# Kernel optimization log

Hardware: AMD Instinct MI355X
Metric: run time of the kernel (lower is better)

## Reference

```python
import jax, jax.numpy as jnp
import numpy as np

BLOCK = 128  # RHT block size (multiple of E8 lattice dim 8)


def _hadamard(n: int) -> np.ndarray:
    """Sylvester Hadamard matrix of size n (n power of 2), unnormalized."""
    H = np.array([[1.0]], dtype=np.float32)
    while H.shape[0] < n:
        H = np.block([[H, H], [H, -H]]).astype(np.float32)
    return H

_H = jnp.asarray(_hadamard(BLOCK) / np.sqrt(BLOCK))  # orthonormal [BLOCK, BLOCK]


def rht(x, signs):
    """Block-diagonal randomized Hadamard transform: x*signs then blockwise H.
    x: [T, D] with D % BLOCK == 0; signs: [D] of +-1."""
    T, D = x.shape
    xs = (x * signs).reshape(T, D // BLOCK, BLOCK)
    return jnp.einsum('tnb,bc->tnc', xs, _H).reshape(T, D)


def e8rht_linear(x, wq, scale, signs):
    """E8RHT quantized linear: rotate input, dequantize weight, matmul.
    wq: [out, in] quantized codes (stored as float), scale: [out] per-row scale."""
    xr = rht(x, signs)                       # [T, in]
    w = wq * scale[:, None]                  # dequantize [out, in]
    return xr @ w.T                          # [T, out]


def setup_inputs() -> dict:
    key = jax.random.key(0)
    ks = jax.random.split(key, 7)
    T, D_IN, D_MID, D_OUT = 16384, 1024, 4096, 1024
    x = jax.random.normal(ks[0], (T, D_IN), dtype=jnp.float32)
    # simulate lattice-quantized codes: small-integer-ish values
    up_wq = jnp.round(jax.random.normal(ks[1], (D_MID, D_IN)) * 2.0)
    up_scale = (jax.random.uniform(ks[2], (D_MID,)) * 0.02 + 0.005).astype(jnp.float32)
    down_wq = jnp.round(jax.random.normal(ks[3], (D_OUT, D_MID)) * 2.0)
    down_scale = (jax.random.uniform(ks[4], (D_OUT,)) * 0.02 + 0.005).astype(jnp.float32)
    up_signs = jnp.sign(jax.random.normal(ks[5], (D_IN,))).astype(jnp.float32)
    down_signs = jnp.sign(jax.random.normal(ks[6], (D_MID,))).astype(jnp.float32)
    return {"x": x, "up_wq": up_wq, "up_scale": up_scale,
            "down_wq": down_wq, "down_scale": down_scale,
            "up_signs": up_signs, "down_signs": down_signs}


def reference(x, up_wq, up_scale, down_wq, down_scale, up_signs, down_signs):
    h = e8rht_linear(x, up_wq, up_scale, up_signs)       # [T, D_MID]
    a = jax.nn.gelu(h)                                    # non-gated activation
    out = e8rht_linear(a, down_wq, down_scale, down_signs)  # [T, D_OUT]
    return out
```

## Files before the change

kernel.cpp:

```cpp
#include <hip/hip_runtime.h>
#include <hip/hip_bf16.h>
#include <stdint.h>


typedef __attribute__((ext_vector_type(8))) short short8;
typedef __attribute__((ext_vector_type(16))) float floatx16;

__device__ __forceinline__ float bf2f(unsigned int u16) {
    union { unsigned int i; float f; } v;
    v.i = u16 << 16;
    return v.f;
}

__device__ __forceinline__ unsigned short f2bf(float f) {
    union { float f; unsigned int i; } v;
    v.f = f;
    unsigned int r = v.i + 0x7FFFu + ((v.i >> 16) & 1u);
    return (unsigned short)(r >> 16);
}

__device__ __forceinline__ float gelu_tanh(float x) {
    float u = 0.7978845608028654f * (x + 0.044715f * x * x * x);
    float e = __expf(2.0f * u);
    float t = 1.0f - 2.0f / (e + 1.0f);
    return 0.5f * x * (1.0f + t);
}

__device__ __forceinline__ int dtype_flag(const void* signs_raw) {
    return ((*(const unsigned int*)signs_raw) & 0xFFFFu) ? 1 : 0;
}

__device__ __forceinline__ void fwht_block(const void* wq, const void* scale,
                                           const void* signs, unsigned short* out,
                                           int fl, int D, int nblk, int gwave, int lane) {
    int o = gwave / nblk;
    int blk = gwave - o * nblk;
    size_t base = (size_t)o * D + (size_t)blk * 128;

    float v0, v1, s0, s1, sc;
    if (fl) {
        unsigned int p = ((const unsigned int*)((const unsigned short*)wq + base))[lane];
        v0 = bf2f(p & 0xffffu);
        v1 = bf2f(p >> 16);
        unsigned int sp =
            ((const unsigned int*)((const unsigned short*)signs + (size_t)blk * 128))[lane];
        s0 = bf2f(sp & 0xffffu);
        s1 = bf2f(sp >> 16);
        sc = bf2f(((const unsigned short*)scale)[o]);
    } else {
        const float* wf = (const float*)wq + base;
        v0 = wf[2 * lane];
        v1 = wf[2 * lane + 1];
        const float* sf = (const float*)signs + (size_t)blk * 128;
        s0 = sf[2 * lane];
        s1 = sf[2 * lane + 1];
        sc = ((const float*)scale)[o];
    }

    {
        float a = v0, b = v1;
        v0 = a + b;
        v1 = a - b;
    }
#pragma unroll
    for (int m = 1; m <= 32; m <<= 1) {
        float p0 = __shfl_xor(v0, m, 64);
        float p1 = __shfl_xor(v1, m, 64);
        if (lane & m) {
            v0 = p0 - v0;
            v1 = p1 - v1;
        } else {
            v0 = v0 + p0;
            v1 = v1 + p1;
        }
    }

    sc *= 0.08838834764831845f;
    unsigned short o0 = f2bf(v0 * sc * s0);
    unsigned short o1 = f2bf(v1 * sc * s1);
    ((unsigned int*)(out + base))[lane] = (unsigned int)o0 | ((unsigned int)o1 << 16);
}

__global__ __launch_bounds__(256) void prep(const void* __restrict__ x,
                                            const void* __restrict__ up_wq,
                                            const void* __restrict__ up_scale,
                                            const void* __restrict__ dn_wq,
                                            const void* __restrict__ dn_scale,
                                            const void* __restrict__ up_signs,
                                            const void* __restrict__ dn_signs,
                                            unsigned short* __restrict__ x_bf,
                                            unsigned short* __restrict__ w_up,
                                            unsigned short* __restrict__ w_dn,
                                            int nbX, int nbW, int D_IN, int D_MID) {
    const int fl = dtype_flag(up_signs);
    const int bid = blockIdx.x;
    if (bid < nbX) {
        size_t e = ((size_t)bid * 256 + threadIdx.x) * 8;
        if (fl) {
            *(uint4*)(x_bf + e) = *(const uint4*)((const unsigned short*)x + e);
        } else {
            const float* xf = (const float*)x + e;
            uint4 r;
            r.x = (unsigned)f2bf(xf[0]) | ((unsigned)f2bf(xf[1]) << 16);
            r.y = (unsigned)f2bf(xf[2]) | ((unsigned)f2bf(xf[3]) << 16);
            r.z = (unsigned)f2bf(xf[4]) | ((unsigned)f2bf(xf[5]) << 16);
            r.w = (unsigned)f2bf(xf[6]) | ((unsigned)f2bf(xf[7]) << 16);
            *(uint4*)(x_bf + e) = r;
        }
    } else if (bid < nbX + nbW) {
        int gwave = (bid - nbX) * 4 + (threadIdx.x >> 6);
        fwht_block(up_wq, up_scale, up_signs, w_up, fl, D_IN, D_IN / 128, gwave,
                   threadIdx.x & 63);
    } else {
        int gwave = (bid - nbX - nbW) * 4 + (threadIdx.x >> 6);
        fwht_block(dn_wq, dn_scale, dn_signs, w_dn, fl, D_MID, D_MID / 128, gwave,
                   threadIdx.x & 63);
    }
}

template <int ACT, int OUT_DYN>
__global__ __launch_bounds__(256, 4) void gemm_bt(const unsigned short* __restrict__ A,
                                                  const unsigned short* __restrict__ B,
                                                  void* __restrict__ C,
                                                  const void* __restrict__ sflag,
                                                  int N, int K, int rowOff,
                                                  int NT, int GM, int strip) {
    __shared__ unsigned short As[128 * 32];
    __shared__ unsigned short Bs[128 * 32];

    int flat = blockIdx.x;
    int mt, nt;
    if (strip > 0) {
        int xcd = flat & 7;
        int s = flat >> 3;
        int perPanel = GM * NT;
        int p = s / perPanel;
        int r = s - p * perPanel;
        nt = r / GM;
        mt = xcd * strip + p * GM + (r - nt * GM);
    } else {
        int perPanel = GM * NT;
        int p = flat / perPanel;
        int r = flat - p * perPanel;
        nt = r / GM;
        mt = p * GM + (r - nt * GM);
    }
    const int tileM = mt * 128;
    const int tileN = nt * 128;

    const int tid = threadIdx.x;
    const int lane = tid & 63;
    const int wave = tid >> 6;
    const int fl = OUT_DYN ? dtype_flag(sflag) : 1;

    const int wm = wave & 1, wn = wave >> 1;
    const int m0 = wm * 64, n0 = wn * 64;

    const int srow = wave * 32 + (lane >> 2);
    const int scol = (((lane & 3) ^ ((srow >> 1) & 3)) * 8);

    floatx16 acc[2][2];
#pragma unroll
    for (int i = 0; i < 2; i++)
#pragma unroll
        for (int j = 0; j < 2; j++) acc[i][j] = (floatx16)0.0f;

    const int r31 = lane & 31;
    const int kg = lane >> 5;
    const int sl0 = kg ^ ((r31 >> 1) & 3);
    const int sl1 = sl0 ^ 2;

    const int eA[2][2] = {
        {(m0 + r31) * 32 + sl0 * 8, (m0 + r31) * 32 + sl1 * 8},
        {(m0 + 32 + r31) * 32 + sl0 * 8, (m0 + 32 + r31) * 32 + sl1 * 8}};
    const int eB[2][2] = {
        {(n0 + r31) * 32 + sl0 * 8, (n0 + r31) * 32 + sl1 * 8},
        {(n0 + 32 + r31) * 32 + sl0 * 8, (n0 + 32 + r31) * 32 + sl1 * 8}};

    const unsigned short* Abase = A + (size_t)(tileM + srow) * K + scol;
    const unsigned short* Bbase = B + (size_t)(tileN + srow) * K + scol;
    unsigned short* AsDst = As + wave * 1024;
    unsigned short* BsDst = Bs + wave * 1024;

    for (int k0 = 0; k0 < K; k0 += 32) {
        __builtin_amdgcn_global_load_lds(
            (const __attribute__((address_space(1))) unsigned int*)(Abase + k0),
            (__attribute__((address_space(3))) unsigned int*)(AsDst), 16, 0, 0);
        __builtin_amdgcn_global_load_lds(
            (const __attribute__((address_space(1))) unsigned int*)(Abase + k0 + (size_t)16 * K),
            (__attribute__((address_space(3))) unsigned int*)(AsDst + 512), 16, 0, 0);
        __builtin_amdgcn_global_load_lds(
            (const __attribute__((address_space(1))) unsigned int*)(Bbase + k0),
            (__attribute__((address_space(3))) unsigned int*)(BsDst), 16, 0, 0);
        __builtin_amdgcn_global_load_lds(
            (const __attribute__((address_space(1))) unsigned int*)(Bbase + k0 + (size_t)16 * K),
            (__attribute__((address_space(3))) unsigned int*)(BsDst + 512), 16, 0, 0);

        __syncthreads();

        short8 af[2][2], bf[2][2];
#pragma unroll
        for (int mi = 0; mi < 2; mi++)
#pragma unroll
            for (int ks = 0; ks < 2; ks++) {
                af[mi][ks] = *(const short8*)&As[eA[mi][ks]];
                bf[mi][ks] = *(const short8*)&Bs[eB[mi][ks]];
            }
#pragma unroll
        for (int mi = 0; mi < 2; mi++)
#pragma unroll
            for (int ni = 0; ni < 2; ni++)
#pragma unroll
                for (int ks = 0; ks < 2; ks++)
                    acc[mi][ni] = __builtin_amdgcn_mfma_f32_32x32x16_bf16(
                        af[mi][ks], bf[ni][ks], acc[mi][ni], 0, 0, 0);
        __syncthreads();
    }

#pragma unroll
    for (int mi = 0; mi < 2; mi++) {
        int rb0 = tileM + m0 + mi * 32 + kg * 4;
#pragma unroll
        for (int ni = 0; ni < 2; ni++) {
            int c = tileN + n0 + ni * 32 + r31;
#pragma unroll
            for (int g = 0; g < 4; g++) {
#pragma unroll
                for (int r = 0; r < 4; r++) {
                    float v = acc[mi][ni][g * 4 + r];
                    if (ACT) v = gelu_tanh(v);
                    size_t idx = (size_t)(rowOff + rb0 + g * 8 + r) * N + c;
                    if (fl)
                        ((unsigned short*)C)[idx] = f2bf(v);
                    else
                        ((float*)C)[idx] = v;
                }
            }
        }
    }
}

static inline int div_le(int n, int cap) {
    for (int g = cap; g > 1; --g)
        if (n % g == 0) return g;
    return 1;
}

extern "C" void kernel_launch(void* const* d_in, const int* in_sizes, int n_in,
                              void* d_out, int out_size, void* d_ws, size_t ws_size,
                              hipStream_t stream) {
    const int T = 16384, D_IN = 1024, D_MID = 4096, D_OUT = 1024;

    unsigned short* w_up = (unsigned short*)d_ws;
    unsigned short* w_dn = w_up + (size_t)D_MID * D_IN;
    unsigned short* x_bf = w_dn + (size_t)D_OUT * D_MID;
    unsigned short* a_buf = x_bf + (size_t)T * D_IN;

    size_t used = ((size_t)D_MID * D_IN + (size_t)D_OUT * D_MID + (size_t)T * D_IN) * 2;
    size_t avail = ws_size > used ? ws_size - used : 0;
    long tc = (long)(avail / ((size_t)D_MID * 2));
    tc = (tc / 128) * 128;
    if (tc > T) tc = T;
    if (tc < 128) tc = 128;
    const int Tc = (int)tc;

    {
        int nbX = (T * D_IN / 8) / 256;
        int nbW = (D_MID * (D_IN / 128)) / 4;
        prep<<<dim3(nbX + 2 * nbW), dim3(256), 0, stream>>>(
            d_in[0], d_in[1], d_in[2], d_in[3], d_in[4], d_in[5], d_in[6], x_bf, w_up, w_dn,
            nbX, nbW, D_IN, D_MID);
    }

    for (int r0 = 0; r0 < T; r0 += Tc) {
        int Ms = (T - r0 < Tc) ? (T - r0) : Tc;
        int MT = Ms / 128;
        int strip = (MT % 8 == 0) ? MT / 8 : 0;

        {
            int NT = D_MID / 128;
            int GM = (strip > 0) ? div_le(strip, 16) : div_le(MT, 4);
            gemm_bt<1, 0><<<dim3(MT * NT), dim3(256), 0, stream>>>(
                x_bf + (size_t)r0 * D_IN, w_up, a_buf, d_in[5], D_MID, D_IN, 0, NT, GM, strip);
        }
        {
            int NT = D_OUT / 128;
            int GM = (strip > 0) ? div_le(strip, 4) : div_le(MT, 4);
            gemm_bt<0, 1><<<dim3(MT * NT), dim3(256), 0, stream>>>(
                a_buf, w_dn, d_out, d_in[5], D_OUT, D_MID, r0, NT, GM, strip);
        }
    }
}
```

Before: 480.0 us.

## Replace 128x128 GEMM with 256x256 double-buffered 8-wave pipelined kernel

Replaces the simple single-buffered 128x128 tile GEMM (4 waves, 32x32 MFMA, BK=32) with a 256x256 tile kernel using 8 waves, 16x16x32 MFMA, BK=64 and double-buffered LDS. Global-to-LDS loads for the next K tile are interleaved between MFMA quadrants, with explicit waitcnt, barriers and setprio. The goal is to raise data reuse per byte loaded and hide load latency behind compute. In exchange it uses more LDS and registers, runs at lower occupancy, launches fewer blocks per GEMM, and relies on hand-placed barriers that are fragile.

Result: faster. 426.0 us (-11.2%).

```diff
diff --git a/kernel.cpp b/kernel.cpp
--- a/kernel.cpp
+++ b/kernel.cpp
@@ -1,10 +1,35 @@
 #include <hip/hip_runtime.h>
-#include <hip/hip_bf16.h>
 #include <stdint.h>
 
 
 typedef __attribute__((ext_vector_type(8))) short short8;
-typedef __attribute__((ext_vector_type(16))) float floatx16;
+typedef __attribute__((ext_vector_type(4))) float floatx4;
+
+#define GLOAD(gp, lp)                                                               \
+  __builtin_amdgcn_global_load_lds(                                                 \
+      (const __attribute__((address_space(1))) unsigned int*)(gp),                  \
+      (__attribute__((address_space(3))) unsigned int*)(lp), 16, 0, 0)
+
+#define SCHED0() __builtin_amdgcn_sched_barrier(0)
+#define BARRIER()                                  \
+  do {                                             \
+    SCHED0();                                      \
+    asm volatile("" ::: "memory");                 \
+    __builtin_amdgcn_s_barrier();                  \
+    asm volatile("" ::: "memory");                 \
+    SCHED0();                                      \
+  } while (0)
+#define LGKM0()                                              \
+  do {                                                       \
+    asm volatile("s_waitcnt lgkmcnt(0)" ::: "memory");       \
+    SCHED0();                                                \
+  } while (0)
+#define LGKM_HINT() asm volatile("s_waitcnt lgkmcnt(8)" ::: "memory")
+#define VMCNT(n)                                             \
+  do {                                                       \
+    asm volatile("s_waitcnt vmcnt(" #n ")" ::: "memory");    \
+    SCHED0();                                                \
+  } while (0)
 
 __device__ __forceinline__ float bf2f(unsigned int u16) {
     union { unsigned int i; float f; } v;
@@ -118,123 +143,180 @@
     }
 }
 
+__device__ __forceinline__ void stage_half(const unsigned short* g, unsigned short* l,
+                                           size_t goff, int K, int ldsW) {
+    GLOAD(g + goff, l + ldsW);
+    GLOAD(g + goff + (size_t)8 * K, l + ldsW + 512);
+}
+
+__device__ __forceinline__ void ld_frags(short8 (&fr)[2][2], const unsigned short* base,
+                                         int o0, int o1) {
+#pragma unroll
+    for (int f = 0; f < 2; ++f) {
+        fr[f][0] = *(const short8*)(base + f * 1024 + o0);
+        fr[f][1] = *(const short8*)(base + f * 1024 + o1);
+    }
+}
+
+__device__ __forceinline__ void ld_frags4(short8 (&fr)[4][2], const unsigned short* base,
+                                          int o0, int o1) {
+#pragma unroll
+    for (int f = 0; f < 4; ++f) {
+        fr[f][0] = *(const short8*)(base + f * 1024 + o0);
+        fr[f][1] = *(const short8*)(base + f * 1024 + o1);
+    }
+}
+
+__device__ __forceinline__ void mfma_quad(floatx4 (&acc)[8][4], const short8 (&ar)[4][2],
+                                          const short8 (&br)[2][2], int MO, int NO) {
+    __builtin_amdgcn_s_setprio(1);
+#pragma unroll
+    for (int ks = 0; ks < 2; ++ks)
+#pragma unroll
+        for (int fm = 0; fm < 4; ++fm)
+#pragma unroll
+            for (int fn = 0; fn < 2; ++fn)
+                acc[MO + fm][NO + fn] = __builtin_amdgcn_mfma_f32_16x16x32_bf16(
+                    ar[fm][ks], br[fn][ks], acc[MO + fm][NO + fn], 0, 0, 0);
+    __builtin_amdgcn_s_setprio(0);
+}
+
 template <int ACT, int OUT_DYN>
-__global__ __launch_bounds__(256, 4) void gemm_bt(const unsigned short* __restrict__ A,
+__global__ __launch_bounds__(512, 2) void gemm256(const unsigned short* __restrict__ A,
                                                   const unsigned short* __restrict__ B,
                                                   void* __restrict__ C,
                                                   const void* __restrict__ sflag,
                                                   int N, int K, int rowOff,
-                                                  int NT, int GM, int strip) {
-    __shared__ unsigned short As[128 * 32];
-    __shared__ unsigned short Bs[128 * 32];
+                                                  int NTn, int GM, int strip) {
+    __shared__ __align__(16) unsigned short As[2][2][128 * 64];
+    __shared__ __align__(16) unsigned short Bs[2][2][128 * 64];
 
     int flat = blockIdx.x;
     int mt, nt;
     if (strip > 0) {
         int xcd = flat & 7;
         int s = flat >> 3;
-        int perPanel = GM * NT;
+        int perPanel = GM * NTn;
         int p = s / perPanel;
         int r = s - p * perPanel;
         nt = r / GM;
         mt = xcd * strip + p * GM + (r - nt * GM);
     } else {
-        int perPanel = GM * NT;
+        int perPanel = GM * NTn;
         int p = flat / perPanel;
         int r = flat - p * perPanel;
         nt = r / GM;
         mt = p * GM + (r - nt * GM);
     }
-    const int tileM = mt * 128;
-    const int tileN = nt * 128;
+    const int tileM = mt * 256, tileN = nt * 256;
 
     const int tid = threadIdx.x;
     const int lane = tid & 63;
     const int wave = tid >> 6;
-    const int fl = OUT_DYN ? dtype_flag(sflag) : 1;
-
-    const int wm = wave & 1, wn = wave >> 1;
-    const int m0 = wm * 64, n0 = wn * 64;
-
-    const int srow = wave * 32 + (lane >> 2);
-    const int scol = (((lane & 3) ^ ((srow >> 1) & 3)) * 8);
-
-    floatx16 acc[2][2];
-#pragma unroll
-    for (int i = 0; i < 2; i++)
-#pragma unroll
-        for (int j = 0; j < 2; j++) acc[i][j] = (floatx16)0.0f;
-
-    const int r31 = lane & 31;
-    const int kg = lane >> 5;
-    const int sl0 = kg ^ ((r31 >> 1) & 3);
-    const int sl1 = sl0 ^ 2;
-
-    const int eA[2][2] = {
-        {(m0 + r31) * 32 + sl0 * 8, (m0 + r31) * 32 + sl1 * 8},
-        {(m0 + 32 + r31) * 32 + sl0 * 8, (m0 + 32 + r31) * 32 + sl1 * 8}};
-    const int eB[2][2] = {
-        {(n0 + r31) * 32 + sl0 * 8, (n0 + r31) * 32 + sl1 * 8},
-        {(n0 + 32 + r31) * 32 + sl0 * 8, (n0 + 32 + r31) * 32 + sl1 * 8}};
-
-    const unsigned short* Abase = A + (size_t)(tileM + srow) * K + scol;
-    const unsigned short* Bbase = B + (size_t)(tileN + srow) * K + scol;
-    unsigned short* AsDst = As + wave * 1024;
-    unsigned short* BsDst = Bs + wave * 1024;
-
-    for (int k0 = 0; k0 < K; k0 += 32) {
-        __builtin_amdgcn_global_load_lds(
-            (const __attribute__((address_space(1))) unsigned int*)(Abase + k0),
-            (__attribute__((address_space(3))) unsigned int*)(AsDst), 16, 0, 0);
-        __builtin_amdgcn_global_load_lds(
-            (const __attribute__((address_space(1))) unsigned int*)(Abase + k0 + (size_t)16 * K),
-            (__attribute__((address_space(3))) unsigned int*)(AsDst + 512), 16, 0, 0);
-        __builtin_amdgcn_global_load_lds(
-            (const __attribute__((address_space(1))) unsigned int*)(Bbase + k0),
-            (__attribute__((address_space(3))) unsigned int*)(BsDst), 16, 0, 0);
-        __builtin_amdgcn_global_load_lds(
-            (const __attribute__((address_space(1))) unsigned int*)(Bbase + k0 + (size_t)16 * K),
-            (__attribute__((address_space(3))) unsigned int*)(BsDst + 512), 16, 0, 0);
-
-        __syncthreads();
-
-        short8 af[2][2], bf[2][2];
-#pragma unroll
-        for (int mi = 0; mi < 2; mi++)
-#pragma unroll
-            for (int ks = 0; ks < 2; ks++) {
-                af[mi][ks] = *(const short8*)&As[eA[mi][ks]];
-                bf[mi][ks] = *(const short8*)&Bs[eB[mi][ks]];
-            }
-#pragma unroll
-        for (int mi = 0; mi < 2; mi++)
-#pragma unroll
-            for (int ni = 0; ni < 2; ni++)
-#pragma unroll
-                for (int ks = 0; ks < 2; ks++)
-                    acc[mi][ni] = __builtin_amdgcn_mfma_f32_32x32x16_bf16(
-                        af[mi][ks], bf[ni][ks], acc[mi][ni], 0, 0, 0);
-        __syncthreads();
-    }
-
-#pragma unroll
-    for (int mi = 0; mi < 2; mi++) {
-        int rb0 = tileM + m0 + mi * 32 + kg * 4;
-#pragma unroll
-        for (int ni = 0; ni < 2; ni++) {
-            int c = tileN + n0 + ni * 32 + r31;
-#pragma unroll
-            for (int g = 0; g < 4; g++) {
-#pragma unroll
-                for (int r = 0; r < 4; r++) {
-                    float v = acc[mi][ni][g * 4 + r];
-                    if (ACT) v = gelu_tanh(v);
-                    size_t idx = (size_t)(rowOff + rb0 + g * 8 + r) * N + c;
-                    if (fl)
-                        ((unsigned short*)C)[idx] = f2bf(v);
-                    else
-                        ((float*)C)[idx] = v;
-                }
+    const int wm = wave >> 2;
+    const int wn = wave & 3;
+
+    int fl = 1;
+    if (OUT_DYN) {
+        fl = dtype_flag(sflag);
+        asm volatile("" ::"v"(fl));
+    }
+
+    const int gcol = (((lane & 7) ^ (lane >> 3)) * 8);
+    const size_t goff = (size_t)(wave * 16 + (lane >> 3)) * K + gcol;
+    const int ldsW = wave * 1024;
+
+    const int sw = (lane & 7) * 8;
+    const int o0 = (lane & 15) * 64 + (((lane >> 4) * 8) ^ sw);
+    const int o1 = (lane & 15) * 64 + ((32 | ((lane >> 4) * 8)) ^ sw);
+
+    const unsigned short* Ab = A + (size_t)tileM * K;
+    const unsigned short* Bb = B + (size_t)tileN * K;
+    const int NTt = K >> 6;
+
+    floatx4 acc[8][4];
+#pragma unroll
+    for (int i = 0; i < 8; ++i)
+#pragma unroll
+        for (int j = 0; j < 4; ++j) acc[i][j] = (floatx4)0.0f;
+
+    stage_half(Ab, &As[0][0][0], goff, K, ldsW);
+    stage_half(Bb, &Bs[0][0][0], goff, K, ldsW);
+    stage_half(Ab + (size_t)128 * K, &As[0][1][0], goff, K, ldsW);
+    stage_half(Bb + (size_t)128 * K, &Bs[0][1][0], goff, K, ldsW);
+    if (NTt > 1) {
+        stage_half(Ab + 64, &As[1][0][0], goff, K, ldsW);
+        stage_half(Bb + 64, &Bs[1][0][0], goff, K, ldsW);
+        VMCNT(4);
+    } else {
+        VMCNT(0);
+    }
+    BARRIER();
+
+    short8 ar0[4][2], ar1[4][2], br0[2][2], br1[2][2];
+
+    for (int t = 0; t < NTt; ++t) {
+        const int d = t & 1, e = d ^ 1;
+        const unsigned short* Ah = &As[d][wm][0];
+        const unsigned short* Bh = &Bs[d][wn >> 1][0];
+        const int bro = (wn & 1) * 64 * 64;
+
+        ld_frags4(ar0, Ah, o0, o1);
+        ld_frags(br0, Bh + bro, o0, o1);
+        if (t + 1 < NTt)
+            stage_half(Ab + (size_t)128 * K + (size_t)(t + 1) * 64, &As[e][1][0], goff, K,
+                       ldsW);
+        LGKM_HINT();
+        BARRIER();
+        LGKM0();
+        mfma_quad(acc, ar0, br0, 0, 0);
+        BARRIER();
+
+        ld_frags4(ar1, Ah + 64 * 64, o0, o1);
+        ld_frags(br1, Bh + bro + 32 * 64, o0, o1);
+        if (t + 1 < NTt)
+            stage_half(Bb + (size_t)128 * K + (size_t)(t + 1) * 64, &Bs[e][1][0], goff, K,
+                       ldsW);
+        LGKM_HINT();
+        BARRIER();
+        LGKM0();
+        mfma_quad(acc, ar1, br0, 4, 0);
+        BARRIER();
+
+        if (t + 2 < NTt)
+            stage_half(Ab + (size_t)(t + 2) * 64, &As[d][0][0], goff, K, ldsW);
+        BARRIER();
+        mfma_quad(acc, ar1, br1, 4, 2);
+        BARRIER();
+
+        if (t + 2 < NTt) {
+            stage_half(Bb + (size_t)(t + 2) * 64, &Bs[d][0][0], goff, K, ldsW);
+            VMCNT(4);
+        } else {
+            VMCNT(0);
+        }
+        BARRIER();
+        mfma_quad(acc, ar0, br1, 0, 2);
+        BARRIER();
+    }
+
+    const int c4 = lane & 15;
+    const int rg = (lane >> 4) * 4;
+#pragma unroll
+    for (int fm = 0; fm < 8; ++fm) {
+        const int gr = tileM + wm * 128 + fm * 16 + rg;
+#pragma unroll
+        for (int fn = 0; fn < 4; ++fn) {
+            const int gc = tileN + wn * 64 + fn * 16 + c4;
+#pragma unroll
+            for (int j = 0; j < 4; ++j) {
+                float v = acc[fm][fn][j];
+                if (ACT) v = gelu_tanh(v);
+                size_t idx = (size_t)(rowOff + gr + j) * N + gc;
+                if (fl)
+                    ((unsigned short*)C)[idx] = f2bf(v);
+                else
+                    ((float*)C)[idx] = v;
             }
         }
     }
@@ -259,9 +341,9 @@
     size_t used = ((size_t)D_MID * D_IN + (size_t)D_OUT * D_MID + (size_t)T * D_IN) * 2;
     size_t avail = ws_size > used ? ws_size - used : 0;
     long tc = (long)(avail / ((size_t)D_MID * 2));
-    tc = (tc / 128) * 128;
+    tc = (tc / 256) * 256;
     if (tc > T) tc = T;
-    if (tc < 128) tc = 128;
+    if (tc < 256) tc = 256;
     const int Tc = (int)tc;
 
     {
@@ -274,20 +356,21 @@
 
     for (int r0 = 0; r0 < T; r0 += Tc) {
         int Ms = (T - r0 < Tc) ? (T - r0) : Tc;
-        int MT = Ms / 128;
-        int strip = (MT % 8 == 0) ? MT / 8 : 0;
+        int MT = Ms / 256;
+        int strip = (MT % 8 == 0 && MT >= 8) ? MT / 8 : 0;
 
         {
-            int NT = D_MID / 128;
-            int GM = (strip > 0) ? div_le(strip, 16) : div_le(MT, 4);
-            gemm_bt<1, 0><<<dim3(MT * NT), dim3(256), 0, stream>>>(
-                x_bf + (size_t)r0 * D_IN, w_up, a_buf, d_in[5], D_MID, D_IN, 0, NT, GM, strip);
+            int NTn = D_MID / 256;
+            int GM = (strip > 0) ? div_le(strip, 4) : div_le(MT, 4);
+            gemm256<1, 0><<<dim3(MT * NTn), dim3(512), 0, stream>>>(
+                x_bf + (size_t)r0 * D_IN, w_up, a_buf, d_in[5], D_MID, D_IN, 0, NTn, GM,
+                strip);
         }
         {
-            int NT = D_OUT / 128;
-            int GM = (strip > 0) ? div_le(strip, 4) : div_le(MT, 4);
-            gemm_bt<0, 1><<<dim3(MT * NT), dim3(256), 0, stream>>>(
-                a_buf, w_dn, d_out, d_in[5], D_OUT, D_MID, r0, NT, GM, strip);
-        }
-    }
-}
+            int NTn = D_OUT / 256;
+            int GM = (strip > 0) ? div_le(strip, 2) : div_le(MT, 2);
+            gemm256<0, 1><<<dim3(MT * NTn), dim3(512), 0, stream>>>(
+                a_buf, w_dn, d_out, d_in[5], D_OUT, D_MID, r0, NTn, GM, strip);
+        }
+    }
+}
```

## Double-buffer GEMM LDS tiles to prefetch next K-slice during MFMA

Applied to the files above, without the earlier changes.

The GEMM kernel now uses two LDS buffers per operand. It issues the global-to-LDS loads for the next K-slice before running the MFMAs on the current one, which leaves one barrier per iteration instead of two. Explicit waitcnt and sched_barrier control and s_setprio around the MFMA block are added. The prep kernel also uses vectorized float2/float4 loads. LDS use doubles to 32KB per block, which may limit occupancy at the declared 4 blocks per CU.

New measurement: 515.8 us. 1.07x slower.

```diff
diff --git a/kernel.cpp b/kernel.cpp
--- a/kernel.cpp
+++ b/kernel.cpp
@@ -1,10 +1,34 @@
 #include <hip/hip_runtime.h>
-#include <hip/hip_bf16.h>
 #include <stdint.h>
 
 
 typedef __attribute__((ext_vector_type(8))) short short8;
 typedef __attribute__((ext_vector_type(16))) float floatx16;
+
+#define GLOAD(gp, lp)                                                               \
+  __builtin_amdgcn_global_load_lds(                                                 \
+      (const __attribute__((address_space(1))) unsigned int*)(gp),                  \
+      (__attribute__((address_space(3))) unsigned int*)(lp), 16, 0, 0)
+
+#define SCHED0() __builtin_amdgcn_sched_barrier(0)
+#define BARRIER()                                  \
+  do {                                             \
+    SCHED0();                                      \
+    asm volatile("" ::: "memory");                 \
+    __builtin_amdgcn_s_barrier();                  \
+    asm volatile("" ::: "memory");                 \
+    SCHED0();                                      \
+  } while (0)
+#define LGKM0()                                              \
+  do {                                                       \
+    asm volatile("s_waitcnt lgkmcnt(0)" ::: "memory");       \
+    SCHED0();                                                \
+  } while (0)
+#define VMCNT0()                                             \
+  do {                                                       \
+    asm volatile("s_waitcnt vmcnt(0)" ::: "memory");         \
+    SCHED0();                                                \
+  } while (0)
 
 __device__ __forceinline__ float bf2f(unsigned int u16) {
     union { unsigned int i; float f; } v;
@@ -48,12 +72,12 @@
         s1 = bf2f(sp >> 16);
         sc = bf2f(((const unsigned short*)scale)[o]);
     } else {
-        const float* wf = (const float*)wq + base;
-        v0 = wf[2 * lane];
-        v1 = wf[2 * lane + 1];
-        const float* sf = (const float*)signs + (size_t)blk * 128;
-        s0 = sf[2 * lane];
-        s1 = sf[2 * lane + 1];
+        const float2 wv = *(const float2*)((const float*)wq + base + 2 * lane);
+        v0 = wv.x;
+        v1 = wv.y;
+        const float2 sv = *(const float2*)((const float*)signs + (size_t)blk * 128 + 2 * lane);
+        s0 = sv.x;
+        s1 = sv.y;
         sc = ((const float*)scale)[o];
     }
 
@@ -100,11 +124,13 @@
             *(uint4*)(x_bf + e) = *(const uint4*)((const unsigned short*)x + e);
         } else {
             const float* xf = (const float*)x + e;
+            float4 a = *(const float4*)(xf);
+            float4 b = *(const float4*)(xf + 4);
             uint4 r;
-            r.x = (unsigned)f2bf(xf[0]) | ((unsigned)f2bf(xf[1]) << 16);
-            r.y = (unsigned)f2bf(xf[2]) | ((unsigned)f2bf(xf[3]) << 16);
-            r.z = (unsigned)f2bf(xf[4]) | ((unsigned)f2bf(xf[5]) << 16);
-            r.w = (unsigned)f2bf(xf[6]) | ((unsigned)f2bf(xf[7]) << 16);
+            r.x = (unsigned)f2bf(a.x) | ((unsigned)f2bf(a.y) << 16);
+            r.y = (unsigned)f2bf(a.z) | ((unsigned)f2bf(a.w) << 16);
+            r.z = (unsigned)f2bf(b.x) | ((unsigned)f2bf(b.y) << 16);
+            r.w = (unsigned)f2bf(b.z) | ((unsigned)f2bf(b.w) << 16);
             *(uint4*)(x_bf + e) = r;
         }
     } else if (bid < nbX + nbW) {
@@ -119,110 +145,124 @@
 }
 
 template <int ACT, int OUT_DYN>
-__global__ __launch_bounds__(256, 4) void gemm_bt(const unsigned short* __restrict__ A,
+__global__ __launch_bounds__(256, 4) void gemm128(const unsigned short* __restrict__ A,
                                                   const unsigned short* __restrict__ B,
                                                   void* __restrict__ C,
                                                   const void* __restrict__ sflag,
                                                   int N, int K, int rowOff,
-                                                  int NT, int GM, int strip) {
-    __shared__ unsigned short As[128 * 32];
-    __shared__ unsigned short Bs[128 * 32];
+                                                  int NTn, int GM, int strip) {
+    __shared__ __align__(16) unsigned short As[2][128 * 32];
+    __shared__ __align__(16) unsigned short Bs[2][128 * 32];
 
     int flat = blockIdx.x;
     int mt, nt;
     if (strip > 0) {
         int xcd = flat & 7;
         int s = flat >> 3;
-        int perPanel = GM * NT;
+        int perPanel = GM * NTn;
         int p = s / perPanel;
         int r = s - p * perPanel;
         nt = r / GM;
         mt = xcd * strip + p * GM + (r - nt * GM);
     } else {
-        int perPanel = GM * NT;
+        int perPanel = GM * NTn;
         int p = flat / perPanel;
         int r = flat - p * perPanel;
         nt = r / GM;
         mt = p * GM + (r - nt * GM);
     }
-    const int tileM = mt * 128;
-    const int tileN = nt * 128;
+    const int tileM = mt * 128, tileN = nt * 128;
 
     const int tid = threadIdx.x;
     const int lane = tid & 63;
     const int wave = tid >> 6;
-    const int fl = OUT_DYN ? dtype_flag(sflag) : 1;
-
-    const int wm = wave & 1, wn = wave >> 1;
-    const int m0 = wm * 64, n0 = wn * 64;
-
-    const int srow = wave * 32 + (lane >> 2);
-    const int scol = (((lane & 3) ^ ((srow >> 1) & 3)) * 8);
-
-    floatx16 acc[2][2];
-#pragma unroll
-    for (int i = 0; i < 2; i++)
-#pragma unroll
-        for (int j = 0; j < 2; j++) acc[i][j] = (floatx16)0.0f;
+    const int wm = wave >> 1;
+    const int wn = wave & 1;
+
+    int fl = 1;
+    if (OUT_DYN) {
+        fl = dtype_flag(sflag);
+        asm volatile("" ::"v"(fl));
+    }
+
+    const int gcol = (((lane & 3) ^ ((lane >> 3) & 3)) * 8);
+    const size_t goff = (size_t)(wave * 32 + (lane >> 2)) * K + gcol;
+    const int ldsOff = wave * 1024;
 
     const int r31 = lane & 31;
     const int kg = lane >> 5;
-    const int sl0 = kg ^ ((r31 >> 1) & 3);
-    const int sl1 = sl0 ^ 2;
-
-    const int eA[2][2] = {
-        {(m0 + r31) * 32 + sl0 * 8, (m0 + r31) * 32 + sl1 * 8},
-        {(m0 + 32 + r31) * 32 + sl0 * 8, (m0 + 32 + r31) * 32 + sl1 * 8}};
-    const int eB[2][2] = {
-        {(n0 + r31) * 32 + sl0 * 8, (n0 + r31) * 32 + sl1 * 8},
-        {(n0 + 32 + r31) * 32 + sl0 * 8, (n0 + 32 + r31) * 32 + sl1 * 8}};
-
-    const unsigned short* Abase = A + (size_t)(tileM + srow) * K + scol;
-    const unsigned short* Bbase = B + (size_t)(tileN + srow) * K + scol;
-    unsigned short* AsDst = As + wave * 1024;
-    unsigned short* BsDst = Bs + wave * 1024;
-
-    for (int k0 = 0; k0 < K; k0 += 32) {
-        __builtin_amdgcn_global_load_lds(
-            (const __attribute__((address_space(1))) unsigned int*)(Abase + k0),
-            (__attribute__((address_space(3))) unsigned int*)(AsDst), 16, 0, 0);
-        __builtin_amdgcn_global_load_lds(
-            (const __attribute__((address_space(1))) unsigned int*)(Abase + k0 + (size_t)16 * K),
-            (__attribute__((address_space(3))) unsigned int*)(AsDst + 512), 16, 0, 0);
-        __builtin_amdgcn_global_load_lds(
-            (const __attribute__((address_space(1))) unsigned int*)(Bbase + k0),
-            (__attribute__((address_space(3))) unsigned int*)(BsDst), 16, 0, 0);
-        __builtin_amdgcn_global_load_lds(
-            (const __attribute__((address_space(1))) unsigned int*)(Bbase + k0 + (size_t)16 * K),
-            (__attribute__((address_space(3))) unsigned int*)(BsDst + 512), 16, 0, 0);
-
-        __syncthreads();
+    const int sw = (r31 >> 1) & 3;
+    const int s0 = ((kg ^ sw)) * 8;
+    const int s1 = s0 ^ 16;
+    const int aBase = (wm * 64 + r31) * 32;
+    const int bBase = (wn * 64 + r31) * 32;
+
+    const unsigned short* Ab = A + (size_t)tileM * K;
+    const unsigned short* Bb = B + (size_t)tileN * K;
+    const int NTt = K >> 5;
+
+    floatx16 acc[2][2];
+#pragma unroll
+    for (int i = 0; i < 2; i++)
+#pragma unroll
+        for (int j = 0; j < 2; j++) acc[i][j] = (floatx16)0.0f;
+
+    GLOAD(Ab + goff, &As[0][ldsOff]);
+    GLOAD(Ab + goff + (size_t)16 * K, &As[0][ldsOff + 512]);
+    GLOAD(Bb + goff, &Bs[0][ldsOff]);
+    GLOAD(Bb + goff + (size_t)16 * K, &Bs[0][ldsOff + 512]);
+    VMCNT0();
+    BARRIER();
+
+    const unsigned short* pA = Ab + goff + 32;
+    const unsigned short* pB = Bb + goff + 32;
+
+    for (int t = 0; t < NTt; ++t) {
+        const int d = t & 1, e = d ^ 1;
+
+        if (t + 1 < NTt) {
+            GLOAD(pA, &As[e][ldsOff]);
+            GLOAD(pA + (size_t)16 * K, &As[e][ldsOff + 512]);
+            GLOAD(pB, &Bs[e][ldsOff]);
+            GLOAD(pB + (size_t)16 * K, &Bs[e][ldsOff + 512]);
+        }
 
         short8 af[2][2], bf[2][2];
-#pragma unroll
-        for (int mi = 0; mi < 2; mi++)
-#pragma unroll
-            for (int ks = 0; ks < 2; ks++) {
-                af[mi][ks] = *(const short8*)&As[eA[mi][ks]];
-                bf[mi][ks] = *(const short8*)&Bs[eB[mi][ks]];
-            }
-#pragma unroll
-        for (int mi = 0; mi < 2; mi++)
-#pragma unroll
-            for (int ni = 0; ni < 2; ni++)
-#pragma unroll
-                for (int ks = 0; ks < 2; ks++)
+        const unsigned short* Ad = &As[d][0];
+        const unsigned short* Bd = &Bs[d][0];
+#pragma unroll
+        for (int rb = 0; rb < 2; ++rb) {
+            af[rb][0] = *(const short8*)(Ad + aBase + rb * 1024 + s0);
+            af[rb][1] = *(const short8*)(Ad + aBase + rb * 1024 + s1);
+            bf[rb][0] = *(const short8*)(Bd + bBase + rb * 1024 + s0);
+            bf[rb][1] = *(const short8*)(Bd + bBase + rb * 1024 + s1);
+        }
+        LGKM0();
+
+        __builtin_amdgcn_s_setprio(1);
+#pragma unroll
+        for (int ks = 0; ks < 2; ++ks)
+#pragma unroll
+            for (int mi = 0; mi < 2; ++mi)
+#pragma unroll
+                for (int ni = 0; ni < 2; ++ni)
                     acc[mi][ni] = __builtin_amdgcn_mfma_f32_32x32x16_bf16(
                         af[mi][ks], bf[ni][ks], acc[mi][ni], 0, 0, 0);
-        __syncthreads();
+        __builtin_amdgcn_s_setprio(0);
+
+        VMCNT0();
+        BARRIER();
+
+        pA += 32;
+        pB += 32;
     }
 
 #pragma unroll
     for (int mi = 0; mi < 2; mi++) {
-        int rb0 = tileM + m0 + mi * 32 + kg * 4;
+        int rb0 = tileM + wm * 64 + mi * 32 + kg * 4;
 #pragma unroll
         for (int ni = 0; ni < 2; ni++) {
-            int c = tileN + n0 + ni * 32 + r31;
+            int c = tileN + wn * 64 + ni * 32 + r31;
 #pragma unroll
             for (int g = 0; g < 4; g++) {
 #pragma unroll
@@ -280,13 +320,14 @@
         {
             int NT = D_MID / 128;
             int GM = (strip > 0) ? div_le(strip, 16) : div_le(MT, 4);
-            gemm_bt<1, 0><<<dim3(MT * NT), dim3(256), 0, stream>>>(
-                x_bf + (size_t)r0 * D_IN, w_up, a_buf, d_in[5], D_MID, D_IN, 0, NT, GM, strip);
+            gemm128<1, 0><<<dim3(MT * NT), dim3(256), 0, stream>>>(
+                x_bf + (size_t)r0 * D_IN, w_up, a_buf, d_in[5], D_MID, D_IN, 0, NT, GM,
+                strip);
         }
         {
             int NT = D_OUT / 128;
             int GM = (strip > 0) ? div_le(strip, 4) : div_le(MT, 4);
-            gemm_bt<0, 1><<<dim3(MT * NT), dim3(256), 0, stream>>>(
+            gemm128<0, 1><<<dim3(MT * NT), dim3(256), 0, stream>>>(
                 a_buf, w_dn, d_out, d_in[5], D_OUT, D_MID, r0, NT, GM, strip);
         }
     }
```
